# Kernel optimization log

Hardware: AMD Instinct MI355X
Metric: run time of the kernel (lower is better)

The kernel has to match this reference:

```python
import jax, jax.numpy as jnp
import numpy as np

K = 1000            # top-k kept per batch element
BG = 0              # background class index
B = 64              # number of batch elements (segments)
NPB = 16384         # candidates per batch element (>= K, equal segments)
C = 80              # number of classes


def setup_inputs() -> dict:
    key = jax.random.key(0)
    k1, k2 = jax.random.split(key)
    scores = jax.random.uniform(k1, (B * NPB, C), dtype=jnp.float32)
    # monotonically rising batch indices, NPB entries per batch
    batch_indices = jnp.repeat(jnp.arange(B, dtype=jnp.int32), NPB)
    boxes = jax.random.normal(k2, (B * NPB, 4), dtype=jnp.float32)
    return {"scores": scores, "batch_indices": batch_indices, "boxes": boxes}


def reference(scores, batch_indices, boxes):
    # foreground score = 1 - P(background)
    fg = 1.0 - scores[:, BG]                         # [N]
    # equal segments -> ragged per-batch top-k == batched top-k
    per_batch = fg.reshape(B, NPB)                   # [B, NPB]
    _, idx = jax.lax.top_k(per_batch, K)             # [B, K] local indices
    offsets = jnp.arange(B, dtype=idx.dtype)[:, None] * NPB
    top_indices = (idx + offsets).reshape(-1)        # [B*K] global indices
    filtered_scores = scores[top_indices]            # [B*K, C]
    filtered_batch_indices = batch_indices[top_indices]  # [B*K]
    filtered_boxes = boxes[top_indices]              # [B*K, 4]
    return (filtered_scores, filtered_batch_indices, filtered_boxes)
```

## Files before the change

kernel.cpp:

```cpp
#include <hip/hip_runtime.h>
#include <stdint.h>

#define BATCHES 64
#define NPB 16384
#define NCLS 80
#define TOPK 1000
#define NTH 1024
#define PER (NPB / NTH)
#define SELCAP 2048

__device__ __forceinline__ uint32_t fg_key(float s) {
    float fg = 1.0f - s;
    if (fg >= 1.0f) return 0xFFFFFFFFu;
    if (fg <= 0.0f) return 0u;
    return (uint32_t)(fg * 4294967296.0f);
}

__global__ __launch_bounds__(256) void key_kernel(const float* __restrict__ scores,
                                                  uint32_t* __restrict__ keys, int n) {
    int gid = blockIdx.x * 256 + threadIdx.x;
    if (gid < n) {
        keys[gid] = fg_key(scores[(size_t)gid * NCLS]);
    }
}

__global__ __launch_bounds__(NTH) void select_kernel(const uint32_t* __restrict__ keys,
                                                     const float* __restrict__ scores,
                                                     const int* __restrict__ batch_indices,
                                                     const float* __restrict__ boxes,
                                                     float* __restrict__ out,
                                                     int have_keys) {
    __shared__ uint32_t hist[256];
    __shared__ uint32_t sfx[256];
    __shared__ uint32_t bc_prefix, bc_rem, selcnt;
    __shared__ unsigned long long sel[SELCAP];

    const int t = threadIdx.x;
    const int b = blockIdx.x;

    uint32_t kreg[PER];
    if (have_keys) {
        const uint32_t* kb = keys + (size_t)b * NPB;
#pragma unroll
        for (int i = 0; i < PER; ++i) kreg[i] = kb[i * NTH + t];
    } else {
#pragma unroll
        for (int i = 0; i < PER; ++i) {
            size_t g = (size_t)b * NPB + (size_t)(i * NTH + t);
            kreg[i] = fg_key(scores[g * NCLS]);
        }
    }

    if (t == 0) { bc_prefix = 0u; bc_rem = TOPK; selcnt = 0u; }
    __syncthreads();

    for (int shift = 24; shift >= 0; shift -= 8) {
        uint32_t prefix = bc_prefix;
        uint32_t rem    = bc_rem;
        uint32_t maskhi = (shift == 24) ? 0u : (0xFFFFFFFFu << (shift + 8));
        if (t < 256) hist[t] = 0u;
        __syncthreads();
#pragma unroll
        for (int i = 0; i < PER; ++i) {
            uint32_t kk = kreg[i];
            if ((kk & maskhi) == prefix) atomicAdd(&hist[(kk >> shift) & 0xFFu], 1u);
        }
        __syncthreads();
        if (t < 256) sfx[t] = hist[t];
        __syncthreads();
        for (int off = 1; off < 256; off <<= 1) {
            uint32_t v = 0u;
            if (t < 256) v = sfx[t] + ((t + off < 256) ? sfx[t + off] : 0u);
            __syncthreads();
            if (t < 256) sfx[t] = v;
            __syncthreads();
        }
        if (t < 256) {
            uint32_t ge = sfx[t];
            uint32_t gt = (t < 255) ? sfx[t + 1] : 0u;
            if (ge >= rem && gt < rem) {
                bc_prefix = prefix | ((uint32_t)t << shift);
                bc_rem = rem - gt;
            }
        }
        __syncthreads();
    }

    const uint32_t pivot = bc_prefix;

#pragma unroll
    for (int i = 0; i < PER; ++i) {
        uint32_t kk = kreg[i];
        if (kk >= pivot) {
            uint32_t pos = atomicAdd(&selcnt, 1u);
            if (pos < SELCAP) {
                uint32_t lidx = (uint32_t)(i * NTH + t);
                sel[pos] = ((unsigned long long)kk << 32) | (unsigned long long)(~lidx);
            }
        }
    }
    __syncthreads();
    const uint32_t M = selcnt;
    for (int i = t; i < SELCAP; i += NTH)
        if ((uint32_t)i >= M) sel[i] = 0ull;
    __syncthreads();

    for (int k2 = 2; k2 <= SELCAP; k2 <<= 1) {
        for (int j = k2 >> 1; j > 0; j >>= 1) {
#pragma unroll
            for (int r = 0; r < SELCAP / NTH; ++r) {
                int i = t + r * NTH;
                int ixj = i ^ j;
                if (ixj > i) {
                    unsigned long long a = sel[i], c = sel[ixj];
                    bool up = ((i & k2) == 0);
                    if ((a < c) == up) { sel[i] = c; sel[ixj] = a; }
                }
            }
            __syncthreads();
        }
    }

    const int wave = t >> 6;
    const int lane = t & 63;
    float* out_scores = out;
    float* out_bi     = out + (size_t)BATCHES * TOPK * NCLS;
    float* out_boxes  = out_bi + (size_t)BATCHES * TOPK;

    for (int j = wave; j < TOPK; j += NTH / 64) {
        unsigned long long e = sel[j];
        uint32_t lidx = ~((uint32_t)e);
        size_t g = (size_t)b * NPB + lidx;
        size_t row = (size_t)b * TOPK + j;
        const float* srow = scores + g * NCLS;
        float* drow = out_scores + row * NCLS;
        if (lane < NCLS) drow[lane] = srow[lane];
        int lane2 = lane + 64;
        if (lane2 < NCLS) drow[lane2] = srow[lane2];
        if (lane < 4) out_boxes[row * 4 + lane] = boxes[g * 4 + lane];
        if (lane == 4) out_bi[row] = (float)batch_indices[g];
    }
}

extern "C" void kernel_launch(void* const* d_in, const int* in_sizes, int n_in,
                              void* d_out, int out_size, void* d_ws, size_t ws_size,
                              hipStream_t stream) {
    const float* scores        = (const float*)d_in[0];
    const int*   batch_indices = (const int*)d_in[1];
    const float* boxes         = (const float*)d_in[2];
    float* out = (float*)d_out;

    const int N = BATCHES * NPB;
    const size_t keys_bytes = (size_t)N * sizeof(uint32_t);

    if (ws_size >= keys_bytes) {
        uint32_t* keys = (uint32_t*)d_ws;
        key_kernel<<<(N + 255) / 256, 256, 0, stream>>>(scores, keys, N);
        select_kernel<<<BATCHES, NTH, 0, stream>>>(keys, scores, batch_indices, boxes, out, 1);
    } else {
        select_kernel<<<BATCHES, NTH, 0, stream>>>(nullptr, scores, batch_indices, boxes, out, 0);
    }
}
```

Measured before the change: 538.9 us.

## Split gather into separate kernel, replace bitonic sort with rank counting

The per-batch selection kernel now swaps the shared-memory bitonic sort for a rank-by-counting pass, replaces the barrier-heavy prefix scan with a wave shuffle scan, and uses ballot-aggregated atomics for compaction. It writes ordered global indices to workspace. A new gather kernel spread over many blocks then copies the score rows with float4 loads and stores. The aim is to stop the output gather from being limited to 64 blocks and to cut barrier-heavy sorting. The cost is an extra launch, and the rank pass does O(M^2) shared-memory reads with no fallback when the workspace is too small.

```diff
diff --git a/kernel.cpp b/kernel.cpp
--- a/kernel.cpp
+++ b/kernel.cpp
@@ -2,12 +2,14 @@
 #include <stdint.h>
 
 #define BATCHES 64
-#define NPB 16384
-#define NCLS 80
-#define TOPK 1000
-#define NTH 1024
-#define PER (NPB / NTH)
-#define SELCAP 2048
+#define NPB     16384
+#define NCLS    80
+#define TOPK    1000
+#define NTH     1024
+#define PER     (NPB / NTH)
+#define SELCAP  2048
+#define GROWS   16
+#define GTH     320
 
 __device__ __forceinline__ uint32_t fg_key(float s) {
     float fg = 1.0f - s;
@@ -17,39 +19,25 @@
 }
 
 __global__ __launch_bounds__(256) void key_kernel(const float* __restrict__ scores,
-                                                  uint32_t* __restrict__ keys, int n) {
+                                                  uint32_t* __restrict__ keys) {
     int gid = blockIdx.x * 256 + threadIdx.x;
-    if (gid < n) {
-        keys[gid] = fg_key(scores[(size_t)gid * NCLS]);
-    }
+    keys[gid] = fg_key(scores[(size_t)gid * NCLS]);
 }
 
 __global__ __launch_bounds__(NTH) void select_kernel(const uint32_t* __restrict__ keys,
-                                                     const float* __restrict__ scores,
-                                                     const int* __restrict__ batch_indices,
-                                                     const float* __restrict__ boxes,
-                                                     float* __restrict__ out,
-                                                     int have_keys) {
-    __shared__ uint32_t hist[256];
-    __shared__ uint32_t sfx[256];
+                                                     int* __restrict__ ordidx) {
+    __shared__ __align__(16) uint32_t hist[256];
     __shared__ uint32_t bc_prefix, bc_rem, selcnt;
-    __shared__ unsigned long long sel[SELCAP];
+    __shared__ __align__(16) unsigned long long sel[SELCAP];
 
     const int t = threadIdx.x;
     const int b = blockIdx.x;
+    const int lane = t & 63;
 
     uint32_t kreg[PER];
-    if (have_keys) {
-        const uint32_t* kb = keys + (size_t)b * NPB;
+    const uint32_t* kb = keys + (size_t)b * NPB;
 #pragma unroll
-        for (int i = 0; i < PER; ++i) kreg[i] = kb[i * NTH + t];
-    } else {
-#pragma unroll
-        for (int i = 0; i < PER; ++i) {
-            size_t g = (size_t)b * NPB + (size_t)(i * NTH + t);
-            kreg[i] = fg_key(scores[g * NCLS]);
-        }
-    }
+    for (int i = 0; i < PER; ++i) kreg[i] = kb[i * NTH + t];
 
     if (t == 0) { bc_prefix = 0u; bc_rem = TOPK; selcnt = 0u; }
     __syncthreads();
@@ -57,30 +45,37 @@
     for (int shift = 24; shift >= 0; shift -= 8) {
         uint32_t prefix = bc_prefix;
         uint32_t rem    = bc_rem;
-        uint32_t maskhi = (shift == 24) ? 0u : (0xFFFFFFFFu << (shift + 8));
         if (t < 256) hist[t] = 0u;
         __syncthreads();
+        uint32_t maskhi = (shift == 24) ? 0u : (0xFFFFFFFFu << (shift + 8));
 #pragma unroll
         for (int i = 0; i < PER; ++i) {
             uint32_t kk = kreg[i];
             if ((kk & maskhi) == prefix) atomicAdd(&hist[(kk >> shift) & 0xFFu], 1u);
         }
         __syncthreads();
-        if (t < 256) sfx[t] = hist[t];
-        __syncthreads();
-        for (int off = 1; off < 256; off <<= 1) {
-            uint32_t v = 0u;
-            if (t < 256) v = sfx[t] + ((t + off < 256) ? sfx[t + off] : 0u);
-            __syncthreads();
-            if (t < 256) sfx[t] = v;
-            __syncthreads();
-        }
-        if (t < 256) {
-            uint32_t ge = sfx[t];
-            uint32_t gt = (t < 255) ? sfx[t + 1] : 0u;
-            if (ge >= rem && gt < rem) {
-                bc_prefix = prefix | ((uint32_t)t << shift);
-                bc_rem = rem - gt;
+        if (t < 64) {
+            uint4 v = ((const uint4*)hist)[lane];
+            uint32_t s3 = v.w;
+            uint32_t s2 = v.z + s3;
+            uint32_t s1 = v.y + s2;
+            uint32_t s0 = v.x + s1;
+            uint32_t x = s0;
+#pragma unroll
+            for (int off = 1; off < 64; off <<= 1) {
+                uint32_t y = (uint32_t)__shfl_down((int)x, off, 64);
+                if (lane + off < 64) x += y;
+            }
+            uint32_t above = x - s0;
+            uint32_t ge[4] = { s0 + above, s1 + above, s2 + above, s3 + above };
+            uint32_t cnt[4] = { v.x, v.y, v.z, v.w };
+#pragma unroll
+            for (int i = 0; i < 4; ++i) {
+                uint32_t gt = ge[i] - cnt[i];
+                if (ge[i] >= rem && gt < rem) {
+                    bc_prefix = prefix | ((uint32_t)(4 * lane + i) << shift);
+                    bc_rem = rem - gt;
+                }
             }
         }
         __syncthreads();
@@ -90,55 +85,67 @@
 
 #pragma unroll
     for (int i = 0; i < PER; ++i) {
-        uint32_t kk = kreg[i];
-        if (kk >= pivot) {
-            uint32_t pos = atomicAdd(&selcnt, 1u);
-            if (pos < SELCAP) {
-                uint32_t lidx = (uint32_t)(i * NTH + t);
-                sel[pos] = ((unsigned long long)kk << 32) | (unsigned long long)(~lidx);
+        bool p = kreg[i] >= pivot;
+        unsigned long long m = __ballot(p);
+        if (m) {
+            int leader = __builtin_ctzll(m);
+            uint32_t cnt = (uint32_t)__popcll(m);
+            uint32_t base = 0;
+            if (lane == leader) base = atomicAdd(&selcnt, cnt);
+            base = (uint32_t)__shfl((int)base, leader, 64);
+            if (p) {
+                uint32_t pos = base + (uint32_t)__popcll(m & ((1ull << lane) - 1ull));
+                if (pos < SELCAP) {
+                    uint32_t lidx = (uint32_t)(i * NTH + t);
+                    sel[pos] = ((unsigned long long)kreg[i] << 32) |
+                               (unsigned long long)(~lidx);
+                }
             }
         }
     }
     __syncthreads();
-    const uint32_t M = selcnt;
-    for (int i = t; i < SELCAP; i += NTH)
-        if ((uint32_t)i >= M) sel[i] = 0ull;
+    uint32_t M = selcnt;
+    if (M > SELCAP) M = SELCAP;
+    if (t < 4 && M + t < SELCAP) sel[M + t] = 0ull;
     __syncthreads();
 
-    for (int k2 = 2; k2 <= SELCAP; k2 <<= 1) {
-        for (int j = k2 >> 1; j > 0; j >>= 1) {
-#pragma unroll
-            for (int r = 0; r < SELCAP / NTH; ++r) {
-                int i = t + r * NTH;
-                int ixj = i ^ j;
-                if (ixj > i) {
-                    unsigned long long a = sel[i], c = sel[ixj];
-                    bool up = ((i & k2) == 0);
-                    if ((a < c) == up) { sel[i] = c; sel[ixj] = a; }
-                }
-            }
-            __syncthreads();
+    const uint32_t Mp = (M + 3u) & ~3u;
+    for (int e = t; e < (int)M; e += NTH) {
+        unsigned long long mine = sel[e];
+        uint32_t r = 0;
+        for (uint32_t j = 0; j < Mp; j += 4) {
+            unsigned long long a0 = sel[j], a1 = sel[j + 1];
+            unsigned long long a2 = sel[j + 2], a3 = sel[j + 3];
+            r += (a0 > mine) + (a1 > mine) + (a2 > mine) + (a3 > mine);
+        }
+        if (r < TOPK) {
+            uint32_t lidx = ~((uint32_t)mine);
+            ordidx[b * TOPK + (int)r] = b * NPB + (int)lidx;
         }
     }
+}
 
-    const int wave = t >> 6;
-    const int lane = t & 63;
+__global__ __launch_bounds__(GTH) void gather_kernel(const float* __restrict__ scores,
+                                                     const int* __restrict__ batch_indices,
+                                                     const float* __restrict__ boxes,
+                                                     const int* __restrict__ ordidx,
+                                                     float* __restrict__ out) {
+    const int t = threadIdx.x;
+    const int r = t / 20;
+    const int q = t % 20;
+    const int row = blockIdx.x * GROWS + r;
+
     float* out_scores = out;
     float* out_bi     = out + (size_t)BATCHES * TOPK * NCLS;
     float* out_boxes  = out_bi + (size_t)BATCHES * TOPK;
 
-    for (int j = wave; j < TOPK; j += NTH / 64) {
-        unsigned long long e = sel[j];
-        uint32_t lidx = ~((uint32_t)e);
-        size_t g = (size_t)b * NPB + lidx;
-        size_t row = (size_t)b * TOPK + j;
-        const float* srow = scores + g * NCLS;
-        float* drow = out_scores + row * NCLS;
-        if (lane < NCLS) drow[lane] = srow[lane];
-        int lane2 = lane + 64;
-        if (lane2 < NCLS) drow[lane2] = srow[lane2];
-        if (lane < 4) out_boxes[row * 4 + lane] = boxes[g * 4 + lane];
-        if (lane == 4) out_bi[row] = (float)batch_indices[g];
+    int g = ordidx[row];
+    const float4* srow = (const float4*)(scores + (size_t)g * NCLS);
+    float4 v = srow[q];
+    ((float4*)(out_scores + (size_t)row * NCLS))[q] = v;
+    if (q == 0) {
+        ((float4*)out_boxes)[row] = ((const float4*)boxes)[g];
+        out_bi[row] = (float)batch_indices[g];
     }
 }
 
@@ -151,13 +158,11 @@
     float* out = (float*)d_out;
 
     const int N = BATCHES * NPB;
-    const size_t keys_bytes = (size_t)N * sizeof(uint32_t);
+    uint32_t* keys = (uint32_t*)d_ws;
+    int* ordidx = (int*)d_ws + N;
 
-    if (ws_size >= keys_bytes) {
-        uint32_t* keys = (uint32_t*)d_ws;
-        key_kernel<<<(N + 255) / 256, 256, 0, stream>>>(scores, keys, N);
-        select_kernel<<<BATCHES, NTH, 0, stream>>>(keys, scores, batch_indices, boxes, out, 1);
-    } else {
-        select_kernel<<<BATCHES, NTH, 0, stream>>>(nullptr, scores, batch_indices, boxes, out, 0);
-    }
+    key_kernel<<<N / 256, 256, 0, stream>>>(scores, keys);
+    select_kernel<<<BATCHES, NTH, 0, stream>>>(keys, ordidx);
+    gather_kernel<<<(BATCHES * TOPK) / GROWS, GTH, 0, stream>>>(
+        scores, batch_indices, boxes, ordidx, out);
 }
```

Result: faster. 446.9 us (-17.1%).
